# Performance work log

Hardware: AMD Instinct MI355X
Metric: run time of the kernel (lower is better)

Reference implementation:

```python
import jax, jax.numpy as jnp
import numpy as np

B, S, D, H = 4, 2048, 1024, 16
HD = D // H  # head_size = 64


def setup_inputs() -> dict:
    key = jax.random.key(0)
    kx, kq, kk, kv = jax.random.split(key, 4)
    scale = 1.0 / np.sqrt(D)
    return {
        "x": jax.random.normal(kx, (B, S, D), dtype=jnp.float32),
        "Wq": jax.random.normal(kq, (H, HD, D), dtype=jnp.float32) * scale,
        "Wk": jax.random.normal(kk, (H, HD, D), dtype=jnp.float32) * scale,
        "Wv": jax.random.normal(kv, (H, HD, D), dtype=jnp.float32) * scale,
    }


def reference(x, Wq, Wk, Wv):
    # Per-head projections (Linear with weight [out, in]: y = x @ W.T),
    # vectorized over heads: [B,S,D] x [H,HD,D] -> [B,H,S,HD]
    q = jnp.einsum('bsd,hed->bhse', x, Wq)
    k = jnp.einsum('bsd,hed->bhse', x, Wk)
    v = jnp.einsum('bsd,hed->bhse', x, Wv)

    # Scaled scores: [B,H,S,S]
    att = jnp.einsum('bhqe,bhke->bhqk', q, k) / jnp.sqrt(jnp.asarray(HD, x.dtype))

    # Causal mask (lower-triangular incl. diagonal)
    causal = jnp.tril(jnp.ones((S, S), dtype=bool))
    att = jnp.where(causal, att, -jnp.inf)
    att = jax.nn.softmax(att, axis=-1)

    # Weighted values, then concat heads along feature dim -> [B,S,D]
    out = jnp.einsum('bhqk,bhke->bhqe', att, v)
    out = out.transpose(0, 2, 1, 3).reshape(B, S, H * HD)
    return out
```

## Files before the change

### kernel.cpp

```cpp
#include <hip/hip_runtime.h>
#include <hip/hip_bf16.h>

#define BATCH 4
#define S_LEN 2048
#define D_DIM 1024
#define NHEAD 16
#define HDIM 64

#define QSCALE 0.18033688011112042f

typedef __attribute__((ext_vector_type(8))) __bf16 bf16x8;
typedef __attribute__((ext_vector_type(4))) __bf16 bf16x4;
typedef __attribute__((ext_vector_type(4))) float f32x4;
typedef __attribute__((ext_vector_type(16))) float f32x16;

static __device__ inline unsigned int bf16_bits(float f) {
    __bf16 h = (__bf16)f;
    return (unsigned int)__builtin_bit_cast(unsigned short, h);
}
static __device__ inline unsigned int pkbf(float a, float b) {
    return bf16_bits(a) | (bf16_bits(b) << 16);
}

#define NX8 1048576
#define NW8 131072

__global__ __launch_bounds__(256) void cvt_all_kernel(
    const float* __restrict__ x,  const float* __restrict__ Wq,
    const float* __restrict__ Wk, const float* __restrict__ Wv,
    __bf16* __restrict__ xb, __bf16* __restrict__ wcat)
{
    const int i = blockIdx.x * 256 + threadIdx.x;
    const float* src;
    __bf16* dst;
    if (i < NX8) {
        src = x + (size_t)i * 8;
        dst = xb + (size_t)i * 8;
    } else {
        const int i2 = i - NX8;
        const int w  = i2 >> 17;
        src = ((w == 0) ? Wq : (w == 1) ? Wk : Wv) + (size_t)(i2 & (NW8 - 1)) * 8;
        dst = wcat + (size_t)i2 * 8;
    }
    const f32x4* p = reinterpret_cast<const f32x4*>(src);
    f32x4 a = p[0], b = p[1];
    bf16x8 r;
    r[0] = (__bf16)a[0]; r[1] = (__bf16)a[1]; r[2] = (__bf16)a[2]; r[3] = (__bf16)a[3];
    r[4] = (__bf16)b[0]; r[5] = (__bf16)b[1]; r[6] = (__bf16)b[2]; r[7] = (__bf16)b[3];
    *reinterpret_cast<bf16x8*>(dst) = r;
}

__global__ __launch_bounds__(256) void proj_gemm_kernel(
    const __bf16* __restrict__ xb, const __bf16* __restrict__ wb,
    __bf16* __restrict__ qo, __bf16* __restrict__ ko, __bf16* __restrict__ vto)
{
    __shared__ __bf16 As[128][32];
    __shared__ __bf16 Bs[128][32];

    const int tid = threadIdx.x;
    const int l  = tid & 63;
    const int w  = tid >> 6;
    const int wm = w >> 1, wn = w & 1;
    const int lr = l & 15, lg = l >> 4, lk = lg * 8;
    const int m0 = blockIdx.y * 128;
    const int n0 = blockIdx.x * 128;
    const int mat = n0 >> 10;
    const int nb  = n0 & 1023;

    const int sr = l >> 2;
    const int sc = (l & 3) * 8;
    const int g0 = w * 2;

    f32x4 acc[4][4] = {};

    for (int d = 0; d < D_DIM; d += 32) {
        __builtin_amdgcn_global_load_lds(
            (const __attribute__((address_space(1))) void*)(xb + (size_t)(m0 + g0 * 16 + sr) * D_DIM + d + sc),
            (__attribute__((address_space(3))) void*)(&As[g0 * 16][0]), 16, 0, 0);
        __builtin_amdgcn_global_load_lds(
            (const __attribute__((address_space(1))) void*)(xb + (size_t)(m0 + (g0 + 1) * 16 + sr) * D_DIM + d + sc),
            (__attribute__((address_space(3))) void*)(&As[(g0 + 1) * 16][0]), 16, 0, 0);
        __builtin_amdgcn_global_load_lds(
            (const __attribute__((address_space(1))) void*)(wb + (size_t)(n0 + g0 * 16 + sr) * D_DIM + d + sc),
            (__attribute__((address_space(3))) void*)(&Bs[g0 * 16][0]), 16, 0, 0);
        __builtin_amdgcn_global_load_lds(
            (const __attribute__((address_space(1))) void*)(wb + (size_t)(n0 + (g0 + 1) * 16 + sr) * D_DIM + d + sc),
            (__attribute__((address_space(3))) void*)(&Bs[(g0 + 1) * 16][0]), 16, 0, 0);
        __syncthreads();

        bf16x8 af[4], bfr[4];
        #pragma unroll
        for (int mi = 0; mi < 4; ++mi)
            af[mi] = *reinterpret_cast<const bf16x8*>(&As[wm * 64 + mi * 16 + lr][lk]);
        #pragma unroll
        for (int ni = 0; ni < 4; ++ni)
            bfr[ni] = *reinterpret_cast<const bf16x8*>(&Bs[wn * 64 + ni * 16 + lr][lk]);
        #pragma unroll
        for (int mi = 0; mi < 4; ++mi) {
            #pragma unroll
            for (int ni = 0; ni < 4; ++ni)
                acc[mi][ni] = __builtin_amdgcn_mfma_f32_16x16x32_bf16(
                    af[mi], bfr[ni], acc[mi][ni], 0, 0, 0);
        }
        __syncthreads();
    }

    const float oscale = (mat == 0) ? QSCALE : 1.0f;
    #pragma unroll
    for (int mi = 0; mi < 4; ++mi) {
        const int mrow = m0 + wm * 64 + mi * 16 + lg * 4;
        const int b = mrow >> 11;
        const int s = mrow & (S_LEN - 1);
        #pragma unroll
        for (int ni = 0; ni < 4; ++ni) {
            const int n = nb + wn * 64 + ni * 16 + lr;
            const int h = n >> 6;
            const int e = n & 63;
            if (mat == 2) {
                bf16x4 pk;
                #pragma unroll
                for (int r = 0; r < 4; ++r) pk[r] = (__bf16)acc[mi][ni][r];
                *reinterpret_cast<bf16x4*>(
                    vto + ((size_t)(b * NHEAD + h) * HDIM + e) * S_LEN + s) = pk;
            } else {
                __bf16* __restrict__ dst = (mat == 0) ? qo : ko;
                #pragma unroll
                for (int r = 0; r < 4; ++r)
                    dst[((size_t)(b * NHEAD + h) * S_LEN + (s + r)) * HDIM + e] =
                        (__bf16)(acc[mi][ni][r] * oscale);
            }
        }
    }
}

template<bool MASK>
__device__ __attribute__((always_inline)) inline void pair_compute(
    int kv0, int qbase, int lq, int lh,
    const __bf16* __restrict__ kp, const __bf16* __restrict__ vp,
    const bf16x8 (&qB)[2][4],
    float (&m_acc)[2], float (&l_lane)[2], f32x16 (&acc)[2][2])
{
    const int kcol = 8 * lh;

    bf16x8 kA[2][4];
    #pragma unroll
    for (int kvb = 0; kvb < 2; ++kvb)
        #pragma unroll
        for (int ks = 0; ks < 4; ++ks)
            kA[kvb][ks] = *reinterpret_cast<const bf16x8*>(
                kp + (size_t)(kv0 + kvb * 32 + lq) * HDIM + ks * 16 + kcol);

    bf16x8 vA[2][4];
    #pragma unroll
    for (int eb = 0; eb < 2; ++eb)
        #pragma unroll
        for (int ks = 0; ks < 4; ++ks)
            vA[eb][ks] = *reinterpret_cast<const bf16x8*>(
                vp + (size_t)(eb * 32 + lq) * S_LEN + kv0 + ks * 16 + kcol);

    #pragma unroll
    for (int t = 0; t < 2; ++t) {
        f32x16 s0 = {}, s1 = {};
        __builtin_amdgcn_s_setprio(1);
        #pragma unroll
        for (int ks = 0; ks < 4; ++ks)
            s0 = __builtin_amdgcn_mfma_f32_32x32x16_bf16(kA[0][ks], qB[t][ks], s0, 0, 0, 0);
        #pragma unroll
        for (int ks = 0; ks < 4; ++ks)
            s1 = __builtin_amdgcn_mfma_f32_32x32x16_bf16(kA[1][ks], qB[t][ks], s1, 0, 0, 0);
        __builtin_amdgcn_s_setprio(0);

        if (MASK) {
            const int qrow = qbase + t * 32 + lq;
            #pragma unroll
            for (int r = 0; r < 16; ++r) {
                const int kvl = (r & 3) + 8 * (r >> 2) + 4 * lh;
                if (kv0 + kvl > qrow)      s0[r] = -1e30f;
                if (kv0 + 32 + kvl > qrow) s1[r] = -1e30f;
            }
        }

        float tm[8];
        #pragma unroll
        for (int r = 0; r < 8; ++r)
            tm[r] = fmaxf(fmaxf(s0[r], s0[r + 8]), fmaxf(s1[r], s1[r + 8]));
        float mx = fmaxf(fmaxf(fmaxf(tm[0], tm[1]), fmaxf(tm[2], tm[3])),
                         fmaxf(fmaxf(tm[4], tm[5]), fmaxf(tm[6], tm[7])));

        if (!__all(mx - m_acc[t] <= 8.0f)) {
            mx = fmaxf(mx, __shfl_xor(mx, 32));
            const float mnew = fmaxf(m_acc[t], mx);
            const float sc = exp2f(m_acc[t] - mnew);
            l_lane[t] *= sc;
            acc[t][0] *= sc;
            acc[t][1] *= sc;
            m_acc[t] = mnew;
        }

        const float mt = m_acc[t];
        float p0[16], p1[16];
        float psum = 0.0f;
        #pragma unroll
        for (int r = 0; r < 16; ++r) { p0[r] = exp2f(s0[r] - mt); psum += p0[r]; }
        #pragma unroll
        for (int r = 0; r < 16; ++r) { p1[r] = exp2f(s1[r] - mt); psum += p1[r]; }
        l_lane[t] += psum;

        bf16x8 pB[4];
        #pragma unroll
        for (int sl = 0; sl < 2; ++sl) {
            const int b = sl * 8;
            {
                unsigned A = pkbf(p0[b + 0], p0[b + 1]);
                unsigned C = pkbf(p0[b + 2], p0[b + 3]);
                unsigned B = pkbf(p0[b + 4], p0[b + 5]);
                unsigned D = pkbf(p0[b + 6], p0[b + 7]);
                auto r0 = __builtin_amdgcn_permlane32_swap((int)A, (int)B, false, false);
                auto r1 = __builtin_amdgcn_permlane32_swap((int)C, (int)D, false, false);
                uint4 u;
                u.x = (unsigned)r0[0]; u.y = (unsigned)r1[0];
                u.z = (unsigned)r0[1]; u.w = (unsigned)r1[1];
                pB[sl] = __builtin_bit_cast(bf16x8, u);
            }
            {
                unsigned A = pkbf(p1[b + 0], p1[b + 1]);
                unsigned C = pkbf(p1[b + 2], p1[b + 3]);
                unsigned B = pkbf(p1[b + 4], p1[b + 5]);
                unsigned D = pkbf(p1[b + 6], p1[b + 7]);
                auto r0 = __builtin_amdgcn_permlane32_swap((int)A, (int)B, false, false);
                auto r1 = __builtin_amdgcn_permlane32_swap((int)C, (int)D, false, false);
                uint4 u;
                u.x = (unsigned)r0[0]; u.y = (unsigned)r1[0];
                u.z = (unsigned)r0[1]; u.w = (unsigned)r1[1];
                pB[2 + sl] = __builtin_bit_cast(bf16x8, u);
            }
        }

        __builtin_amdgcn_s_setprio(1);
        #pragma unroll
        for (int eb = 0; eb < 2; ++eb)
            #pragma unroll
            for (int ks = 0; ks < 4; ++ks)
                acc[t][eb] = __builtin_amdgcn_mfma_f32_32x32x16_bf16(
                    vA[eb][ks], pB[ks], acc[t][eb], 0, 0, 0);
        __builtin_amdgcn_s_setprio(0);
    }
}

__global__ __launch_bounds__(64, 1) void attn_kernel(
    const __bf16* __restrict__ q, const __bf16* __restrict__ k,
    const __bf16* __restrict__ vt, float* __restrict__ out)
{
    const int l  = threadIdx.x;
    const int lq = l & 31;
    const int lh = l >> 5;
    const int kcol = 8 * lh;

    const int n   = blockIdx.x;
    const int xcd = n & 7;
    const int m   = n >> 3;
    const int tp  = m >> 3;
    const int bh  = xcd * 8 + (m & 7);

    const __bf16* __restrict__ kp = k  + (size_t)bh * S_LEN * HDIM;
    const __bf16* __restrict__ vp = vt + (size_t)bh * HDIM * S_LEN;
    const int bq = bh >> 4;
    const int hq = bh & 15;

    #pragma unroll 1
    for (int ph = 0; ph < 2; ++ph) {
        const int qq    = ph ? (31 - tp) : tp;
        const int qbase = qq * 64;
        const int iters = qq + 1;

        const __bf16* __restrict__ qp = q + ((size_t)bh * S_LEN + qbase) * HDIM;
        bf16x8 qB[2][4];
        #pragma unroll
        for (int t = 0; t < 2; ++t)
            #pragma unroll
            for (int ks = 0; ks < 4; ++ks)
                qB[t][ks] = *reinterpret_cast<const bf16x8*>(
                    qp + (size_t)(t * 32 + lq) * HDIM + ks * 16 + kcol);

        float m_acc[2], l_lane[2];
        f32x16 acc[2][2] = {};
        #pragma unroll
        for (int t = 0; t < 2; ++t) { m_acc[t] = -1e30f; l_lane[t] = 0.0f; }

        #pragma unroll 1
        for (int j = 0; j < iters - 1; ++j)
            pair_compute<false>(j * 64, qbase, lq, lh, kp, vp,
                                qB, m_acc, l_lane, acc);
        pair_compute<true>((iters - 1) * 64, qbase, lq, lh, kp, vp,
                           qB, m_acc, l_lane, acc);

        #pragma unroll
        for (int t = 0; t < 2; ++t) {
            float lt = l_lane[t];
            lt += __shfl_xor(lt, 32);
            const float liv = 1.0f / lt;
            float* orow = out + (size_t)(bq * S_LEN + qbase + t * 32 + lq) * D_DIM + hq * HDIM;
            #pragma unroll
            for (int eb = 0; eb < 2; ++eb) {
                #pragma unroll
                for (int g = 0; g < 4; ++g) {
                    f32x4 ox;
                    #pragma unroll
                    for (int r = 0; r < 4; ++r) ox[r] = acc[t][eb][g * 4 + r] * liv;
                    *reinterpret_cast<f32x4*>(orow + eb * 32 + g * 8 + 4 * lh) = ox;
                }
            }
        }
    }
}

extern "C" void kernel_launch(void* const* d_in, const int* in_sizes, int n_in,
                              void* d_out, int out_size, void* d_ws, size_t ws_size,
                              hipStream_t stream)
{
    const float* x  = (const float*)d_in[0];
    const float* Wq = (const float*)d_in[1];
    const float* Wk = (const float*)d_in[2];
    const float* Wv = (const float*)d_in[3];
    float* out = (float*)d_out;

    const size_t x_elems = (size_t)BATCH * S_LEN * D_DIM;
    __bf16* xb   = (__bf16*)d_out;
    __bf16* wcat = xb + x_elems;

    const size_t per_buf = (size_t)BATCH * NHEAD * S_LEN * HDIM;
    __bf16* qb = (__bf16*)d_ws;
    __bf16* kb = qb + per_buf;
    __bf16* vb = kb + per_buf;

    cvt_all_kernel<<<dim3((NX8 + 3 * NW8) / 256), dim3(256), 0, stream>>>(
        x, Wq, Wk, Wv, xb, wcat);

    dim3 grid1(3 * D_DIM / 128, (BATCH * S_LEN) / 128);
    proj_gemm_kernel<<<grid1, dim3(256), 0, stream>>>(xb, wcat, qb, kb, vb);

    attn_kernel<<<dim3(1024), dim3(64), 0, stream>>>(qb, kb, vb, out);
}
```

Before: 166.6 us.

## Split KV loop across two waves per block with LDS softmax merge

The attention kernel now runs two wavefronts per block. Each wave handles alternate 64-key tiles of the causal range for the same 64-query tile, and the partial max, sum and output accumulators are merged through shared memory at the end. The goal is more parallelism and latency hiding per query tile, since each block previously ran a single wave. In exchange it adds LDS traffic, two barriers per phase and extra exp/merge arithmetic, and it raises per-block register and LDS pressure.

```diff
diff --git a/kernel.cpp b/kernel.cpp
--- a/kernel.cpp
+++ b/kernel.cpp
@@ -247,11 +247,57 @@
     }
 }
 
-__global__ __launch_bounds__(64, 1) void attn_kernel(
+template<int T>
+__device__ __attribute__((always_inline)) inline void expose_tile(
+    float* region, int l, const float (&m_acc)[2], const float (&lt)[2],
+    const f32x16 (&acc)[2][2])
+{
+    float* p = region + l * 35;
+    p[0] = m_acc[T];
+    p[1] = lt[T];
+    #pragma unroll
+    for (int eb = 0; eb < 2; ++eb)
+        #pragma unroll
+        for (int r = 0; r < 16; ++r)
+            p[2 + eb * 16 + r] = acc[T][eb][r];
+}
+
+template<int T>
+__device__ __attribute__((always_inline)) inline void merge_out(
+    const float* region, int l, int lh, const float (&m_acc)[2],
+    const float (&lt)[2], const f32x16 (&acc)[2][2], float* orow)
+{
+    const float* p = region + l * 35;
+    const float mo = p[0];
+    const float lo = p[1];
+    const float mn = fmaxf(m_acc[T], mo);
+    const float s_own = exp2f(m_acc[T] - mn);
+    const float s_oth = exp2f(mo - mn);
+    const float liv = 1.0f / (lt[T] * s_own + lo * s_oth);
+    #pragma unroll
+    for (int eb = 0; eb < 2; ++eb) {
+        #pragma unroll
+        for (int g = 0; g < 4; ++g) {
+            f32x4 ox;
+            #pragma unroll
+            for (int r = 0; r < 4; ++r) {
+                const float oth = p[2 + eb * 16 + g * 4 + r];
+                ox[r] = (acc[T][eb][g * 4 + r] * s_own + oth * s_oth) * liv;
+            }
+            *reinterpret_cast<f32x4*>(orow + eb * 32 + g * 8 + 4 * lh) = ox;
+        }
+    }
+}
+
+__global__ __launch_bounds__(128, 2) void attn_kernel(
     const __bf16* __restrict__ q, const __bf16* __restrict__ k,
     const __bf16* __restrict__ vt, float* __restrict__ out)
 {
-    const int l  = threadIdx.x;
+    __shared__ float mlds[2 * 64 * 35];
+
+    const int tid = threadIdx.x;
+    const int l  = tid & 63;
+    const int w  = tid >> 6;
     const int lq = l & 31;
     const int lh = l >> 5;
     const int kcol = 8 * lh;
@@ -271,7 +317,7 @@
     for (int ph = 0; ph < 2; ++ph) {
         const int qq    = ph ? (31 - tp) : tp;
         const int qbase = qq * 64;
-        const int iters = qq + 1;
+        const int nkv   = qq + 1;
 
         const __bf16* __restrict__ qp = q + ((size_t)bh * S_LEN + qbase) * HDIM;
         bf16x8 qB[2][4];
@@ -288,29 +334,31 @@
         for (int t = 0; t < 2; ++t) { m_acc[t] = -1e30f; l_lane[t] = 0.0f; }
 
         #pragma unroll 1
-        for (int j = 0; j < iters - 1; ++j)
+        for (int j = w; j < nkv - 1; j += 2)
             pair_compute<false>(j * 64, qbase, lq, lh, kp, vp,
                                 qB, m_acc, l_lane, acc);
-        pair_compute<true>((iters - 1) * 64, qbase, lq, lh, kp, vp,
-                           qB, m_acc, l_lane, acc);
-
-        #pragma unroll
-        for (int t = 0; t < 2; ++t) {
-            float lt = l_lane[t];
-            lt += __shfl_xor(lt, 32);
-            const float liv = 1.0f / lt;
-            float* orow = out + (size_t)(bq * S_LEN + qbase + t * 32 + lq) * D_DIM + hq * HDIM;
-            #pragma unroll
-            for (int eb = 0; eb < 2; ++eb) {
-                #pragma unroll
-                for (int g = 0; g < 4; ++g) {
-                    f32x4 ox;
-                    #pragma unroll
-                    for (int r = 0; r < 4; ++r) ox[r] = acc[t][eb][g * 4 + r] * liv;
-                    *reinterpret_cast<f32x4*>(orow + eb * 32 + g * 8 + 4 * lh) = ox;
-                }
-            }
-        }
+        if (((nkv - 1) & 1) == w)
+            pair_compute<true>((nkv - 1) * 64, qbase, lq, lh, kp, vp,
+                               qB, m_acc, l_lane, acc);
+
+        float lt[2];
+        lt[0] = l_lane[0] + __shfl_xor(l_lane[0], 32);
+        lt[1] = l_lane[1] + __shfl_xor(l_lane[1], 32);
+
+        float* myreg = mlds + w * (64 * 35);
+        if (w == 0) expose_tile<1>(myreg, l, m_acc, lt, acc);
+        else        expose_tile<0>(myreg, l, m_acc, lt, acc);
+        __syncthreads();
+
+        const float* other = mlds + (1 - w) * (64 * 35);
+        if (w == 0) {
+            float* orow = out + (size_t)(bq * S_LEN + qbase + 0 * 32 + lq) * D_DIM + hq * HDIM;
+            merge_out<0>(other, l, lh, m_acc, lt, acc, orow);
+        } else {
+            float* orow = out + (size_t)(bq * S_LEN + qbase + 1 * 32 + lq) * D_DIM + hq * HDIM;
+            merge_out<1>(other, l, lh, m_acc, lt, acc, orow);
+        }
+        __syncthreads();
     }
 }
 
@@ -339,5 +387,5 @@
     dim3 grid1(3 * D_DIM / 128, (BATCH * S_LEN) / 128);
     proj_gemm_kernel<<<grid1, dim3(256), 0, stream>>>(xb, wcat, qb, kb, vb);
 
-    attn_kernel<<<dim3(1024), dim3(64), 0, stream>>>(qb, kb, vb, out);
-}
+    attn_kernel<<<dim3(1024), dim3(128), 0, stream>>>(qb, kb, vb, out);
+}
```

Result: faster. 157.4 us (-5.5%).
